# Kernel optimization log

Hardware: AMD Instinct MI355X
Metric: run time of the kernel (lower is better)

The kernel has to match this reference:

```python
import jax, jax.numpy as jnp
import numpy as np

T, B, D, R = 1024, 32, 1024, 128

def _orth_cols(key, n, r):
    # mimic torch QR-based orthogonal init: Q[:, :r] of a random [n, r] matrix
    a = jax.random.normal(key, (n, r), dtype=jnp.float32)
    q, _ = jnp.linalg.qr(a)
    return q[:, :r]

def setup_inputs() -> dict:
    key = jax.random.key(0)
    ks = jax.random.split(key, 8)
    x = jax.random.normal(ks[0], (T, B, D), dtype=jnp.float32)
    z = jax.random.normal(ks[1], (T, B, D), dtype=jnp.float32)
    h0 = jnp.zeros((B, D), dtype=jnp.float32)
    U_h = _orth_cols(ks[2], D, R)
    V_h = _orth_cols(ks[3], D, R).T  # [R, D] with orthonormal rows
    U_x = _orth_cols(ks[4], D, R)
    V_x = _orth_cols(ks[5], D, R).T
    s_h = jnp.ones((R,), dtype=jnp.float32)
    s_x = jnp.ones((R,), dtype=jnp.float32)
    b = jnp.zeros((D,), dtype=jnp.float32)
    return {"x": x, "z": z, "h0": h0, "U_h": U_h, "V_h": V_h, "s_h": s_h,
            "U_x": U_x, "V_x": V_x, "s_x": s_x, "b": b}

def reference(x, z, h0, U_h, V_h, s_h, U_x, V_x, s_x, b):
    # Precompute V_x @ x_t for all timesteps: [T, B, R]
    Vx_all = jnp.einsum('tbd,rd->tbr', x, V_x)
    Ux_all = jnp.einsum('tbr,dr->tbd', s_x * Vx_all, U_x)  # input branch, no recurrence

    def step(h_prev, inp):
        Ux_t, z_t = inp
        Vh = h_prev @ V_h.T                 # [B, R]
        Uh = (s_h * Vh) @ U_h.T             # [B, D]
        h_new = jnp.tanh(Uh + Ux_t + b)
        out_t = h_new * jax.nn.silu(z_t)
        return h_new, (h_new, out_t)

    _, (hs, output) = jax.lax.scan(step, h0, (Ux_all, z))
    h = jnp.concatenate([h0[None], hs], axis=0)  # [T+1, B, D]
    return output, h
```

## Files before the change

### kernel.cpp

```cpp
#include <hip/hip_runtime.h>
#include <cstdint>

#define T_STEPS 1024
#define BATCH   32
#define DIM     1024
#define RANK    128
#define BD      (BATCH*DIM)
#define TBD     ((size_t)T_STEPS*BD)

typedef _Float16 half2v __attribute__((ext_vector_type(2)));

__device__ __forceinline__ float dot2f(uint32_t a, uint32_t b, float acc) {
#if __has_builtin(__builtin_amdgcn_fdot2)
  return __builtin_amdgcn_fdot2(__builtin_bit_cast(half2v, a),
                                __builtin_bit_cast(half2v, b), acc, false);
#else
  half2v xx = __builtin_bit_cast(half2v, a);
  half2v yy = __builtin_bit_cast(half2v, b);
  return acc + (float)xx[0]*(float)yy[0] + (float)xx[1]*(float)yy[1];
#endif
}

__device__ __forceinline__ float dot2x4(uint4 w, uint4 h, float acc) {
  acc = dot2f(w.x, h.x, acc); acc = dot2f(w.y, h.y, acc);
  acc = dot2f(w.z, h.z, acc); acc = dot2f(w.w, h.w, acc);
  return acc;
}

__device__ __forceinline__ uint16_t f16b(float x) {
  _Float16 h = (_Float16)x;
  return __builtin_bit_cast(unsigned short, h);
}
__device__ __forceinline__ uint32_t pack2(float a, float b) {
  return (uint32_t)f16b(a) | ((uint32_t)f16b(b) << 16);
}
__device__ __forceinline__ float fast_tanh(float x) {
  float e = __expf(2.0f*x);
  return 1.0f - 2.0f/(e + 1.0f);
}
__device__ __forceinline__ float fast_silu(float zz) {
  return zz / (1.0f + __expf(-zz));
}

__device__ __forceinline__ void pin4(uint4 &v) {
  asm volatile("" : "+v"(v.x), "+v"(v.y), "+v"(v.z), "+v"(v.w));
}

template<int K>
__device__ __forceinline__ uint32_t qbcast(uint32_t v) {
  return (uint32_t)__builtin_amdgcn_mov_dpp((int)v, K*0x55, 0xf, 0xf, true);
}
template<int K>
__device__ __forceinline__ uint4 qbcast4(uint4 v) {
  uint4 r;
  r.x = qbcast<K>(v.x); r.y = qbcast<K>(v.y);
  r.z = qbcast<K>(v.z); r.w = qbcast<K>(v.w);
  return r;
}
template<int CTRL>
__device__ __forceinline__ float dpp_xorf(float v) {
  int t = __builtin_amdgcn_mov_dpp(__builtin_bit_cast(int, v), CTRL, 0xf, 0xf, true);
  return __builtin_bit_cast(float, t);
}

__device__ __forceinline__ void lds_barrier() {
  asm volatile("s_waitcnt lgkmcnt(0)" ::: "memory");
  __builtin_amdgcn_s_barrier();
  __builtin_amdgcn_sched_barrier(0);
}

__global__ void prep_kernel(const float* __restrict__ Uh, const float* __restrict__ Vh,
                            const float* __restrict__ sh, const float* __restrict__ Ux,
                            const float* __restrict__ Vx, const float* __restrict__ sx,
                            const float* __restrict__ h0, uint32_t* __restrict__ ws32,
                            float* __restrict__ hout) {
  int i = blockIdx.x*blockDim.x + threadIdx.x;
  int n = gridDim.x*blockDim.x;
  for (int p = i; p < 65536; p += n) {
    int r = p >> 9, dp = p & 511;
    ws32[p] = pack2(Vh[r*1024 + 2*dp], Vh[r*1024 + 2*dp + 1]);
  }
  for (int p = i; p < 65536; p += n) {
    int d = p >> 6, k = p & 63;
    uint32_t w = pack2(Uh[d*128 + k]      * sh[k],
                       Uh[d*128 + 64 + k] * sh[64 + k]);
    if (k < 52) {
      int J = (k >> 2) + 13*(d & 1);
      ws32[65536 + J*2048 + (d >> 1)*4 + (k & 3)] = w;
    } else {
      ws32[118784 + d*12 + (k - 52)] = w;
    }
  }
  for (int p = i; p < 65536; p += n) {
    int r = p >> 9, dp = p & 511;
    ws32[131072 + p] = pack2(Vx[r*1024 + 2*dp], Vx[r*1024 + 2*dp + 1]);
  }
  for (int p = i; p < 65536; p += n) {
    int d = p >> 6, rp = p & 63;
    ws32[196608 + p] = pack2(Ux[d*128 + 2*rp]   * sx[2*rp],
                             Ux[d*128 + 2*rp+1] * sx[2*rp+1]);
  }
  for (int p = i; p < BD; p += n) hout[p] = h0[p];
}

__global__ __launch_bounds__(512, 4) void inp_kernel(
    const float* __restrict__ x, const uint32_t* __restrict__ ws32,
    const float* __restrict__ bias, float* __restrict__ hout) {
  const int t = blockIdx.x;
  const int l = threadIdx.x;
  __shared__ __attribute__((aligned(16))) uint32_t xs[32*516];
  __shared__ __attribute__((aligned(16))) uint16_t svx[BATCH*RANK];

  const float4* xg = (const float4*)(x + (size_t)t*BD);
  #pragma unroll
  for (int k = 0; k < 16; k++) {
    int i = l + 512*k;
    float4 v = xg[i];
    int bb = i >> 8;
    int d4 = i & 255;
    xs[bb*516 + d4*2]     = pack2(v.x, v.y);
    xs[bb*516 + d4*2 + 1] = pack2(v.z, v.w);
  }
  __syncthreads();

  const int q4 = l & 3;
  const int r  = l >> 2;
  const uint4* wrow = (const uint4*)(ws32 + 131072 + r*512);
  float acc0[8], acc1[8];
  #pragma unroll
  for (int bi = 0; bi < 8; bi++) { acc0[bi] = 0.f; acc1[bi] = 0.f; }
  #pragma unroll 4
  for (int J = 0; J < 128; J += 2) {
    uint4 w0 = wrow[J];
    uint4 w1 = wrow[J+1];
    #pragma unroll
    for (int bi = 0; bi < 8; bi++) {
      const uint4* xrow = (const uint4*)(xs + (4*bi + q4)*516);
      uint4 h0v = xrow[J];
      acc0[bi] = dot2f(w0.x, h0v.x, acc0[bi]);
      acc0[bi] = dot2f(w0.y, h0v.y, acc0[bi]);
      acc0[bi] = dot2f(w0.z, h0v.z, acc0[bi]);
      acc0[bi] = dot2f(w0.w, h0v.w, acc0[bi]);
      uint4 h1v = xrow[J+1];
      acc1[bi] = dot2f(w1.x, h1v.x, acc1[bi]);
      acc1[bi] = dot2f(w1.y, h1v.y, acc1[bi]);
      acc1[bi] = dot2f(w1.z, h1v.z, acc1[bi]);
      acc1[bi] = dot2f(w1.w, h1v.w, acc1[bi]);
    }
  }
  #pragma unroll
  for (int bi = 0; bi < 8; bi++)
    svx[(4*bi + q4)*RANK + r] = f16b(acc0[bi] + acc1[bi]);
  __syncthreads();

  const uint4* svx4 = (const uint4*)svx;
  float accb[BATCH];
  #pragma unroll 1
  for (int dd = 0; dd < 2; dd++) {
    int d = l + dd*512;
    const uint4* urow = (const uint4*)(ws32 + 196608 + d*64);
    #pragma unroll
    for (int bi = 0; bi < BATCH; bi++) accb[bi] = 0.f;
    #pragma unroll
    for (int RP = 0; RP < 16; RP++) {
      uint4 w = urow[RP];
      #pragma unroll
      for (int bi = 0; bi < BATCH; bi++) {
        uint4 sv = svx4[bi*16 + RP];
        accb[bi] = dot2f(w.x, sv.x, accb[bi]);
        accb[bi] = dot2f(w.y, sv.y, accb[bi]);
        accb[bi] = dot2f(w.z, sv.z, accb[bi]);
        accb[bi] = dot2f(w.w, sv.w, accb[bi]);
      }
    }
    float bv = bias[d];
    float* cslot = hout + (size_t)(t+1)*BD + d;
    #pragma unroll
    for (int bi = 0; bi < BATCH; bi++)
      cslot[(size_t)bi*DIM] = accb[bi] + bv;
  }
}

__global__ __attribute__((amdgpu_flat_work_group_size(512, 512),
                          amdgpu_waves_per_eu(2, 2)))
void rec_kernel(
    const uint32_t* __restrict__ ws32, const float* __restrict__ z,
    float* __restrict__ outb) {
  const int b  = blockIdx.x;
  const int l  = threadIdx.x;
  const int W  = l & 31;
  const int R8 = l >> 5;
  const int m  = l & 3;
  float* hout = outb + TBD;
  const uint4* vhw4  = (const uint4*)ws32;
  const uint4* uqs4  = (const uint4*)(ws32 + 65536);
  const uint4* ures4 = (const uint4*)(ws32 + 118784);

  __shared__ __attribute__((aligned(16))) uint4    vlds[6144];
  __shared__ __attribute__((aligned(16))) uint4    ulds[3072];
  __shared__ __attribute__((aligned(16))) uint4    hbuf[32*5];
  __shared__ __attribute__((aligned(16))) uint32_t svh32[64];

  uint4 vw[5][4];
  #pragma unroll
  for (int r = 0; r < 5; r++) {
    #pragma unroll
    for (int c = 0; c < 4; c++) vw[r][c] = vhw4[(8*R8 + r)*128 + W*4 + c];
  }
  #pragma unroll
  for (int r = 0; r < 5; r++) {
    #pragma unroll
    for (int c = 0; c < 4; c++) pin4(vw[r][c]);
  }
  #pragma unroll
  for (int rr = 0; rr < 3; rr++) {
    #pragma unroll
    for (int c = 0; c < 4; c++)
      vlds[R8*384 + rr*128 + c*32 + W] = vhw4[(8*R8 + 5 + rr)*128 + W*4 + c];
  }
  #pragma unroll
  for (int j = 0; j < 3; j++) {
    ulds[j*512 + l]     = ures4[(2*l)*3 + j];
    ulds[(3+j)*512 + l] = ures4[(2*l+1)*3 + j];
  }
  uint4 uq0[13], uq1[13];
  #pragma unroll
  for (int J = 0; J < 13; J++) {
    uq0[J] = uqs4[J*512 + l];
    uq1[J] = uqs4[(13+J)*512 + l];
  }
  {
    const float2 v = ((const float2*)(hout + (size_t)b*DIM))[l];
    ((uint32_t*)hbuf)[20*(l>>4) + (l&15)] = pack2(v.x, v.y);
  }
  __syncthreads();

  const float2* zp2 = (const float2*)(z + (size_t)b*DIM) + l;
  float2*       cp2 = (float2*)(hout + BD + (size_t)b*DIM) + l;
  float2*       op2 = (float2*)(outb + (size_t)b*DIM) + l;
  const uint4*  hb4  = hbuf + W*5;
  const uint4*  svh4 = (const uint4*)svh32;
  const int vbase = R8*384;

  #pragma unroll 1
  for (int t = 0; t < T_STEPS; t++) {
    float2 cc = *cp2;
    float2 zz = *zp2;

    float a[8] = {0.f,0.f,0.f,0.f,0.f,0.f,0.f,0.f};
    #pragma unroll
    for (int c = 0; c < 4; c++) {
      uint4 hvc = hb4[c];
      uint4 vA = vlds[vbase + c*32 + W];
      uint4 vB = vlds[vbase + 128 + c*32 + W];
      uint4 vC = vlds[vbase + 256 + c*32 + W];
      a[0] = dot2x4(vw[0][c], hvc, a[0]);
      a[1] = dot2x4(vw[1][c], hvc, a[1]);
      a[2] = dot2x4(vw[2][c], hvc, a[2]);
      a[3] = dot2x4(vw[3][c], hvc, a[3]);
      a[4] = dot2x4(vw[4][c], hvc, a[4]);
      a[5] = dot2x4(vA, hvc, a[5]);
      a[6] = dot2x4(vB, hvc, a[6]);
      a[7] = dot2x4(vC, hvc, a[7]);
    }
    float b4[4];
    {
      const bool s0 = (W & 1);
      #pragma unroll
      for (int i = 0; i < 4; i++) {
        float keep = s0 ? a[2*i+1] : a[2*i];
        float send = s0 ? a[2*i]   : a[2*i+1];
        b4[i] = keep + dpp_xorf<0xB1>(send);
      }
    }
    float c2[2];
    {
      const bool s1 = (W >> 1) & 1;
      #pragma unroll
      for (int i = 0; i < 2; i++) {
        float keep = s1 ? b4[2*i+1] : b4[2*i];
        float send = s1 ? b4[2*i]   : b4[2*i+1];
        c2[i] = keep + dpp_xorf<0x4E>(send);
      }
    }
    float s;
    {
      const bool s2 = (W >> 2) & 1;
      float keep = s2 ? c2[1] : c2[0];
      float send = s2 ? c2[0] : c2[1];
      s = keep + __shfl_xor(send, 4);
    }
    s += __shfl_xor(s, 8);
    s += __shfl_xor(s, 16);
    if (W < 8) {
      int row = 8*R8 + W;
      int idx = ((row & 63) << 1) | (row >> 6);
      ((uint16_t*)svh32)[idx] = f16b(s);
    }
    lds_barrier();

    float p0 = 0.f, p1 = 0.f;
    {
      uint4 svm = svh4[m];
      uint4 sv;
      sv = qbcast4<0>(svm); p0 = dot2x4(uq0[0], sv, p0); p1 = dot2x4(uq1[0], sv, p1);
      sv = qbcast4<1>(svm); p0 = dot2x4(uq0[1], sv, p0); p1 = dot2x4(uq1[1], sv, p1);
      sv = qbcast4<2>(svm); p0 = dot2x4(uq0[2], sv, p0); p1 = dot2x4(uq1[2], sv, p1);
      sv = qbcast4<3>(svm); p0 = dot2x4(uq0[3], sv, p0); p1 = dot2x4(uq1[3], sv, p1);
    }
    {
      uint4 svm = svh4[4 + m];
      uint4 sv;
      sv = qbcast4<0>(svm); p0 = dot2x4(uq0[4], sv, p0); p1 = dot2x4(uq1[4], sv, p1);
      sv = qbcast4<1>(svm); p0 = dot2x4(uq0[5], sv, p0); p1 = dot2x4(uq1[5], sv, p1);
      sv = qbcast4<2>(svm); p0 = dot2x4(uq0[6], sv, p0); p1 = dot2x4(uq1[6], sv, p1);
      sv = qbcast4<3>(svm); p0 = dot2x4(uq0[7], sv, p0); p1 = dot2x4(uq1[7], sv, p1);
    }
    {
      uint4 svm = svh4[8 + m];
      uint4 sv;
      sv = qbcast4<0>(svm); p0 = dot2x4(uq0[8],  sv, p0); p1 = dot2x4(uq1[8],  sv, p1);
      sv = qbcast4<1>(svm); p0 = dot2x4(uq0[9],  sv, p0); p1 = dot2x4(uq1[9],  sv, p1);
      sv = qbcast4<2>(svm); p0 = dot2x4(uq0[10], sv, p0); p1 = dot2x4(uq1[10], sv, p1);
      sv = qbcast4<3>(svm); p0 = dot2x4(uq0[11], sv, p0); p1 = dot2x4(uq1[11], sv, p1);
    }
    {
      uint4 u0b = ulds[0*512 + l], u0c = ulds[1*512 + l], u0d = ulds[2*512 + l];
      uint4 u1b = ulds[3*512 + l], u1c = ulds[4*512 + l], u1d = ulds[5*512 + l];
      uint4 svm = svh4[12 + m];
      uint4 sv;
      sv = qbcast4<0>(svm); p0 = dot2x4(uq0[12], sv, p0); p1 = dot2x4(uq1[12], sv, p1);
      sv = qbcast4<1>(svm); p0 = dot2x4(u0b, sv, p0); p1 = dot2x4(u1b, sv, p1);
      sv = qbcast4<2>(svm); p0 = dot2x4(u0c, sv, p0); p1 = dot2x4(u1c, sv, p1);
      sv = qbcast4<3>(svm); p0 = dot2x4(u0d, sv, p0); p1 = dot2x4(u1d, sv, p1);
    }

    float hv0 = fast_tanh(p0 + cc.x);
    float hv1 = fast_tanh(p1 + cc.y);
    *cp2 = make_float2(hv0, hv1);
    ((uint32_t*)hbuf)[20*(l>>4) + (l&15)] = pack2(hv0, hv1);
    *op2 = make_float2(hv0 * fast_silu(zz.x), hv1 * fast_silu(zz.y));
    lds_barrier();

    cp2 += BD/2; zp2 += BD/2; op2 += BD/2;
  }
}

extern "C" void kernel_launch(void* const* d_in, const int* in_sizes, int n_in,
                              void* d_out, int out_size, void* d_ws, size_t ws_size,
                              hipStream_t stream) {
  const float* x  = (const float*)d_in[0];
  const float* z  = (const float*)d_in[1];
  const float* h0 = (const float*)d_in[2];
  const float* Uh = (const float*)d_in[3];
  const float* Vh = (const float*)d_in[4];
  const float* sh = (const float*)d_in[5];
  const float* Ux = (const float*)d_in[6];
  const float* Vx = (const float*)d_in[7];
  const float* sx = (const float*)d_in[8];
  const float* bb = (const float*)d_in[9];
  float* outb = (float*)d_out;
  uint32_t* ws32 = (uint32_t*)d_ws;

  prep_kernel<<<512, 256, 0, stream>>>(Uh, Vh, sh, Ux, Vx, sx, h0, ws32, outb + TBD);
  inp_kernel<<<T_STEPS, 512, 0, stream>>>(x, ws32, bb, outb + TBD);
  rec_kernel<<<BATCH, 512, 0, stream>>>(ws32, z, outb);
}
```

Measured before the change: 2.468 ms.

## Fuse input projection and recurrence into one persistent kernel with per-step flags

Merges the input-projection kernel and the recurrent kernel into a single launch. Blocks 0-31 run the recurrence while the other 224 blocks compute the input branch per timestep and publish completion through global release/acquire flags, so the recurrence can start before the whole input projection finishes. The recurrent loop also prefetches the next step's input term and replaces the DPP quad-broadcast with direct LDS reads of the reduced vector. The scheme relies on all 256 blocks being co-resident; otherwise the spin-waits could deadlock. It also adds polling traffic on the flags.

```diff
diff --git a/kernel.cpp b/kernel.cpp
--- a/kernel.cpp
+++ b/kernel.cpp
@@ -7,6 +7,7 @@
 #define RANK    128
 #define BD      (BATCH*DIM)
 #define TBD     ((size_t)T_STEPS*BD)
+#define WSP_FLAG 262144
 
 typedef _Float16 half2v __attribute__((ext_vector_type(2)));
 
@@ -46,17 +47,6 @@
   asm volatile("" : "+v"(v.x), "+v"(v.y), "+v"(v.z), "+v"(v.w));
 }
 
-template<int K>
-__device__ __forceinline__ uint32_t qbcast(uint32_t v) {
-  return (uint32_t)__builtin_amdgcn_mov_dpp((int)v, K*0x55, 0xf, 0xf, true);
-}
-template<int K>
-__device__ __forceinline__ uint4 qbcast4(uint4 v) {
-  uint4 r;
-  r.x = qbcast<K>(v.x); r.y = qbcast<K>(v.y);
-  r.z = qbcast<K>(v.z); r.w = qbcast<K>(v.w);
-  return r;
-}
 template<int CTRL>
 __device__ __forceinline__ float dpp_xorf(float v) {
   int t = __builtin_amdgcn_mov_dpp(__builtin_bit_cast(int, v), CTRL, 0xf, 0xf, true);
@@ -101,248 +91,263 @@
                              Ux[d*128 + 2*rp+1] * sx[2*rp+1]);
   }
   for (int p = i; p < BD; p += n) hout[p] = h0[p];
-}
-
-__global__ __launch_bounds__(512, 4) void inp_kernel(
-    const float* __restrict__ x, const uint32_t* __restrict__ ws32,
-    const float* __restrict__ bias, float* __restrict__ hout) {
-  const int t = blockIdx.x;
-  const int l = threadIdx.x;
-  __shared__ __attribute__((aligned(16))) uint32_t xs[32*516];
-  __shared__ __attribute__((aligned(16))) uint16_t svx[BATCH*RANK];
-
-  const float4* xg = (const float4*)(x + (size_t)t*BD);
-  #pragma unroll
-  for (int k = 0; k < 16; k++) {
-    int i = l + 512*k;
-    float4 v = xg[i];
-    int bb = i >> 8;
-    int d4 = i & 255;
-    xs[bb*516 + d4*2]     = pack2(v.x, v.y);
-    xs[bb*516 + d4*2 + 1] = pack2(v.z, v.w);
-  }
-  __syncthreads();
-
-  const int q4 = l & 3;
-  const int r  = l >> 2;
-  const uint4* wrow = (const uint4*)(ws32 + 131072 + r*512);
-  float acc0[8], acc1[8];
-  #pragma unroll
-  for (int bi = 0; bi < 8; bi++) { acc0[bi] = 0.f; acc1[bi] = 0.f; }
-  #pragma unroll 4
-  for (int J = 0; J < 128; J += 2) {
-    uint4 w0 = wrow[J];
-    uint4 w1 = wrow[J+1];
-    #pragma unroll
-    for (int bi = 0; bi < 8; bi++) {
-      const uint4* xrow = (const uint4*)(xs + (4*bi + q4)*516);
-      uint4 h0v = xrow[J];
-      acc0[bi] = dot2f(w0.x, h0v.x, acc0[bi]);
-      acc0[bi] = dot2f(w0.y, h0v.y, acc0[bi]);
-      acc0[bi] = dot2f(w0.z, h0v.z, acc0[bi]);
-      acc0[bi] = dot2f(w0.w, h0v.w, acc0[bi]);
-      uint4 h1v = xrow[J+1];
-      acc1[bi] = dot2f(w1.x, h1v.x, acc1[bi]);
-      acc1[bi] = dot2f(w1.y, h1v.y, acc1[bi]);
-      acc1[bi] = dot2f(w1.z, h1v.z, acc1[bi]);
-      acc1[bi] = dot2f(w1.w, h1v.w, acc1[bi]);
-    }
-  }
-  #pragma unroll
-  for (int bi = 0; bi < 8; bi++)
-    svx[(4*bi + q4)*RANK + r] = f16b(acc0[bi] + acc1[bi]);
-  __syncthreads();
-
-  const uint4* svx4 = (const uint4*)svx;
-  float accb[BATCH];
-  #pragma unroll 1
-  for (int dd = 0; dd < 2; dd++) {
-    int d = l + dd*512;
-    const uint4* urow = (const uint4*)(ws32 + 196608 + d*64);
-    #pragma unroll
-    for (int bi = 0; bi < BATCH; bi++) accb[bi] = 0.f;
-    #pragma unroll
-    for (int RP = 0; RP < 16; RP++) {
-      uint4 w = urow[RP];
-      #pragma unroll
-      for (int bi = 0; bi < BATCH; bi++) {
-        uint4 sv = svx4[bi*16 + RP];
-        accb[bi] = dot2f(w.x, sv.x, accb[bi]);
-        accb[bi] = dot2f(w.y, sv.y, accb[bi]);
-        accb[bi] = dot2f(w.z, sv.z, accb[bi]);
-        accb[bi] = dot2f(w.w, sv.w, accb[bi]);
-      }
-    }
-    float bv = bias[d];
-    float* cslot = hout + (size_t)(t+1)*BD + d;
-    #pragma unroll
-    for (int bi = 0; bi < BATCH; bi++)
-      cslot[(size_t)bi*DIM] = accb[bi] + bv;
-  }
+  for (int p = i; p < 1056; p += n) ws32[WSP_FLAG + p] = 0;
 }
 
 __global__ __attribute__((amdgpu_flat_work_group_size(512, 512),
                           amdgpu_waves_per_eu(2, 2)))
-void rec_kernel(
-    const uint32_t* __restrict__ ws32, const float* __restrict__ z,
-    float* __restrict__ outb) {
-  const int b  = blockIdx.x;
-  const int l  = threadIdx.x;
-  const int W  = l & 31;
-  const int R8 = l >> 5;
-  const int m  = l & 3;
+void fused_kernel(uint32_t* __restrict__ ws32, const float* __restrict__ x,
+                  const float* __restrict__ z, const float* __restrict__ bias,
+                  float* __restrict__ outb) {
+  __shared__ __attribute__((aligned(16))) uint8_t smem[150272];
+  const int g = blockIdx.x;
+  const int l = threadIdx.x;
   float* hout = outb + TBD;
-  const uint4* vhw4  = (const uint4*)ws32;
-  const uint4* uqs4  = (const uint4*)(ws32 + 65536);
-  const uint4* ures4 = (const uint4*)(ws32 + 118784);
-
-  __shared__ __attribute__((aligned(16))) uint4    vlds[6144];
-  __shared__ __attribute__((aligned(16))) uint4    ulds[3072];
-  __shared__ __attribute__((aligned(16))) uint4    hbuf[32*5];
-  __shared__ __attribute__((aligned(16))) uint32_t svh32[64];
-
-  uint4 vw[5][4];
-  #pragma unroll
-  for (int r = 0; r < 5; r++) {
-    #pragma unroll
-    for (int c = 0; c < 4; c++) vw[r][c] = vhw4[(8*R8 + r)*128 + W*4 + c];
-  }
-  #pragma unroll
-  for (int r = 0; r < 5; r++) {
-    #pragma unroll
-    for (int c = 0; c < 4; c++) pin4(vw[r][c]);
-  }
-  #pragma unroll
-  for (int rr = 0; rr < 3; rr++) {
-    #pragma unroll
-    for (int c = 0; c < 4; c++)
-      vlds[R8*384 + rr*128 + c*32 + W] = vhw4[(8*R8 + 5 + rr)*128 + W*4 + c];
-  }
-  #pragma unroll
-  for (int j = 0; j < 3; j++) {
-    ulds[j*512 + l]     = ures4[(2*l)*3 + j];
-    ulds[(3+j)*512 + l] = ures4[(2*l+1)*3 + j];
-  }
-  uint4 uq0[13], uq1[13];
-  #pragma unroll
-  for (int J = 0; J < 13; J++) {
-    uq0[J] = uqs4[J*512 + l];
-    uq1[J] = uqs4[(13+J)*512 + l];
-  }
-  {
-    const float2 v = ((const float2*)(hout + (size_t)b*DIM))[l];
-    ((uint32_t*)hbuf)[20*(l>>4) + (l&15)] = pack2(v.x, v.y);
-  }
-  __syncthreads();
-
-  const float2* zp2 = (const float2*)(z + (size_t)b*DIM) + l;
-  float2*       cp2 = (float2*)(hout + BD + (size_t)b*DIM) + l;
-  float2*       op2 = (float2*)(outb + (size_t)b*DIM) + l;
-  const uint4*  hb4  = hbuf + W*5;
-  const uint4*  svh4 = (const uint4*)svh32;
-  const int vbase = R8*384;
-
-  #pragma unroll 1
-  for (int t = 0; t < T_STEPS; t++) {
+  uint32_t* flags = ws32 + WSP_FLAG;
+
+  if (g < 32) {
+    const int b  = g;
+    const int W  = l & 31;
+    const int R8 = l >> 5;
+    const uint4* vhw4  = (const uint4*)ws32;
+    const uint4* uqs4  = (const uint4*)(ws32 + 65536);
+    const uint4* ures4 = (const uint4*)(ws32 + 118784);
+
+    uint4*    vlds  = (uint4*)smem;
+    uint4*    ulds  = (uint4*)(smem + 98304);
+    uint32_t* hbuf  = (uint32_t*)(smem + 147456);
+    uint32_t* svh32 = (uint32_t*)(smem + 150016);
+
+    uint4 vw[5][4];
+    #pragma unroll
+    for (int r = 0; r < 5; r++) {
+      #pragma unroll
+      for (int c = 0; c < 4; c++) vw[r][c] = vhw4[(8*R8 + r)*128 + W*4 + c];
+    }
+    #pragma unroll
+    for (int r = 0; r < 5; r++) {
+      #pragma unroll
+      for (int c = 0; c < 4; c++) pin4(vw[r][c]);
+    }
+    #pragma unroll
+    for (int rr = 0; rr < 3; rr++) {
+      #pragma unroll
+      for (int c = 0; c < 4; c++)
+        vlds[R8*384 + rr*128 + c*32 + W] = vhw4[(8*R8 + 5 + rr)*128 + W*4 + c];
+    }
+    #pragma unroll
+    for (int j = 0; j < 3; j++) {
+      ulds[j*512 + l]     = ures4[(2*l)*3 + j];
+      ulds[(3+j)*512 + l] = ures4[(2*l+1)*3 + j];
+    }
+    uint4 uq0[13], uq1[13];
+    #pragma unroll
+    for (int J = 0; J < 13; J++) {
+      uq0[J] = uqs4[J*512 + l];
+      uq1[J] = uqs4[(13+J)*512 + l];
+    }
+    {
+      const float2 v = ((const float2*)(hout + (size_t)b*DIM))[l];
+      hbuf[20*(l>>4) + (l&15)] = pack2(v.x, v.y);
+    }
+    __syncthreads();
+
+    const float2* zp2 = (const float2*)(z + (size_t)b*DIM) + l;
+    float2*       cp2 = (float2*)(hout + BD + (size_t)b*DIM) + l;
+    float2*       op2 = (float2*)(outb + (size_t)b*DIM) + l;
+    const uint4*  hb4  = (const uint4*)hbuf + W*5;
+    const uint4*  svh4 = (const uint4*)svh32;
+    const int vbase = R8*384;
+
+    while (__hip_atomic_load(&flags[1], __ATOMIC_ACQUIRE,
+                             __HIP_MEMORY_SCOPE_AGENT) == 0) {}
     float2 cc = *cp2;
-    float2 zz = *zp2;
-
-    float a[8] = {0.f,0.f,0.f,0.f,0.f,0.f,0.f,0.f};
-    #pragma unroll
-    for (int c = 0; c < 4; c++) {
-      uint4 hvc = hb4[c];
-      uint4 vA = vlds[vbase + c*32 + W];
-      uint4 vB = vlds[vbase + 128 + c*32 + W];
-      uint4 vC = vlds[vbase + 256 + c*32 + W];
-      a[0] = dot2x4(vw[0][c], hvc, a[0]);
-      a[1] = dot2x4(vw[1][c], hvc, a[1]);
-      a[2] = dot2x4(vw[2][c], hvc, a[2]);
-      a[3] = dot2x4(vw[3][c], hvc, a[3]);
-      a[4] = dot2x4(vw[4][c], hvc, a[4]);
-      a[5] = dot2x4(vA, hvc, a[5]);
-      a[6] = dot2x4(vB, hvc, a[6]);
-      a[7] = dot2x4(vC, hvc, a[7]);
-    }
-    float b4[4];
-    {
-      const bool s0 = (W & 1);
-      #pragma unroll
-      for (int i = 0; i < 4; i++) {
-        float keep = s0 ? a[2*i+1] : a[2*i];
-        float send = s0 ? a[2*i]   : a[2*i+1];
-        b4[i] = keep + dpp_xorf<0xB1>(send);
-      }
-    }
-    float c2[2];
-    {
-      const bool s1 = (W >> 1) & 1;
-      #pragma unroll
-      for (int i = 0; i < 2; i++) {
-        float keep = s1 ? b4[2*i+1] : b4[2*i];
-        float send = s1 ? b4[2*i]   : b4[2*i+1];
-        c2[i] = keep + dpp_xorf<0x4E>(send);
-      }
-    }
-    float s;
-    {
-      const bool s2 = (W >> 2) & 1;
-      float keep = s2 ? c2[1] : c2[0];
-      float send = s2 ? c2[0] : c2[1];
-      s = keep + __shfl_xor(send, 4);
-    }
-    s += __shfl_xor(s, 8);
-    s += __shfl_xor(s, 16);
-    if (W < 8) {
-      int row = 8*R8 + W;
-      int idx = ((row & 63) << 1) | (row >> 6);
-      ((uint16_t*)svh32)[idx] = f16b(s);
-    }
-    lds_barrier();
-
-    float p0 = 0.f, p1 = 0.f;
-    {
-      uint4 svm = svh4[m];
-      uint4 sv;
-      sv = qbcast4<0>(svm); p0 = dot2x4(uq0[0], sv, p0); p1 = dot2x4(uq1[0], sv, p1);
-      sv = qbcast4<1>(svm); p0 = dot2x4(uq0[1], sv, p0); p1 = dot2x4(uq1[1], sv, p1);
-      sv = qbcast4<2>(svm); p0 = dot2x4(uq0[2], sv, p0); p1 = dot2x4(uq1[2], sv, p1);
-      sv = qbcast4<3>(svm); p0 = dot2x4(uq0[3], sv, p0); p1 = dot2x4(uq1[3], sv, p1);
-    }
-    {
-      uint4 svm = svh4[4 + m];
-      uint4 sv;
-      sv = qbcast4<0>(svm); p0 = dot2x4(uq0[4], sv, p0); p1 = dot2x4(uq1[4], sv, p1);
-      sv = qbcast4<1>(svm); p0 = dot2x4(uq0[5], sv, p0); p1 = dot2x4(uq1[5], sv, p1);
-      sv = qbcast4<2>(svm); p0 = dot2x4(uq0[6], sv, p0); p1 = dot2x4(uq1[6], sv, p1);
-      sv = qbcast4<3>(svm); p0 = dot2x4(uq0[7], sv, p0); p1 = dot2x4(uq1[7], sv, p1);
-    }
-    {
-      uint4 svm = svh4[8 + m];
-      uint4 sv;
-      sv = qbcast4<0>(svm); p0 = dot2x4(uq0[8],  sv, p0); p1 = dot2x4(uq1[8],  sv, p1);
-      sv = qbcast4<1>(svm); p0 = dot2x4(uq0[9],  sv, p0); p1 = dot2x4(uq1[9],  sv, p1);
-      sv = qbcast4<2>(svm); p0 = dot2x4(uq0[10], sv, p0); p1 = dot2x4(uq1[10], sv, p1);
-      sv = qbcast4<3>(svm); p0 = dot2x4(uq0[11], sv, p0); p1 = dot2x4(uq1[11], sv, p1);
-    }
-    {
-      uint4 u0b = ulds[0*512 + l], u0c = ulds[1*512 + l], u0d = ulds[2*512 + l];
-      uint4 u1b = ulds[3*512 + l], u1c = ulds[4*512 + l], u1d = ulds[5*512 + l];
-      uint4 svm = svh4[12 + m];
-      uint4 sv;
-      sv = qbcast4<0>(svm); p0 = dot2x4(uq0[12], sv, p0); p1 = dot2x4(uq1[12], sv, p1);
-      sv = qbcast4<1>(svm); p0 = dot2x4(u0b, sv, p0); p1 = dot2x4(u1b, sv, p1);
-      sv = qbcast4<2>(svm); p0 = dot2x4(u0c, sv, p0); p1 = dot2x4(u1c, sv, p1);
-      sv = qbcast4<3>(svm); p0 = dot2x4(u0d, sv, p0); p1 = dot2x4(u1d, sv, p1);
-    }
-
-    float hv0 = fast_tanh(p0 + cc.x);
-    float hv1 = fast_tanh(p1 + cc.y);
-    *cp2 = make_float2(hv0, hv1);
-    ((uint32_t*)hbuf)[20*(l>>4) + (l&15)] = pack2(hv0, hv1);
-    *op2 = make_float2(hv0 * fast_silu(zz.x), hv1 * fast_silu(zz.y));
-    lds_barrier();
-
-    cp2 += BD/2; zp2 += BD/2; op2 += BD/2;
+
+    #pragma unroll 1
+    for (int t = 0; t < T_STEPS; t++) {
+      float2 zz = *zp2;
+      float2 ccn = make_float2(0.f, 0.f);
+      if (t < T_STEPS - 1) {
+        while (__hip_atomic_load(&flags[t+2], __ATOMIC_ACQUIRE,
+                                 __HIP_MEMORY_SCOPE_AGENT) == 0) {}
+        ccn = cp2[BD/2];
+      }
+
+      float a[8] = {0.f,0.f,0.f,0.f,0.f,0.f,0.f,0.f};
+      #pragma unroll
+      for (int c = 0; c < 4; c++) {
+        uint4 hvc = hb4[c];
+        uint4 vA = vlds[vbase + c*32 + W];
+        uint4 vB = vlds[vbase + 128 + c*32 + W];
+        uint4 vC = vlds[vbase + 256 + c*32 + W];
+        a[0] = dot2x4(vw[0][c], hvc, a[0]);
+        a[1] = dot2x4(vw[1][c], hvc, a[1]);
+        a[2] = dot2x4(vw[2][c], hvc, a[2]);
+        a[3] = dot2x4(vw[3][c], hvc, a[3]);
+        a[4] = dot2x4(vw[4][c], hvc, a[4]);
+        a[5] = dot2x4(vA, hvc, a[5]);
+        a[6] = dot2x4(vB, hvc, a[6]);
+        a[7] = dot2x4(vC, hvc, a[7]);
+      }
+      float b4[4];
+      {
+        const bool s0 = (W & 1);
+        #pragma unroll
+        for (int i = 0; i < 4; i++) {
+          float keep = s0 ? a[2*i+1] : a[2*i];
+          float send = s0 ? a[2*i]   : a[2*i+1];
+          b4[i] = keep + dpp_xorf<0xB1>(send);
+        }
+      }
+      float c2[2];
+      {
+        const bool s1 = (W >> 1) & 1;
+        #pragma unroll
+        for (int i = 0; i < 2; i++) {
+          float keep = s1 ? b4[2*i+1] : b4[2*i];
+          float send = s1 ? b4[2*i]   : b4[2*i+1];
+          c2[i] = keep + dpp_xorf<0x4E>(send);
+        }
+      }
+      float s;
+      {
+        const bool s2 = (W >> 2) & 1;
+        float keep = s2 ? c2[1] : c2[0];
+        float send = s2 ? c2[0] : c2[1];
+        s = keep + __shfl_xor(send, 4);
+      }
+      s += __shfl_xor(s, 8);
+      s += __shfl_xor(s, 16);
+      if (W < 8) {
+        int row = 8*R8 + W;
+        int idx = ((row & 63) << 1) | (row >> 6);
+        ((uint16_t*)svh32)[idx] = f16b(s);
+      }
+      lds_barrier();
+
+      float p0 = 0.f, p1 = 0.f;
+      {
+        uint4 sv0 = svh4[0], sv1 = svh4[1], sv2 = svh4[2], sv3 = svh4[3];
+        p0 = dot2x4(uq0[0], sv0, p0); p1 = dot2x4(uq1[0], sv0, p1);
+        p0 = dot2x4(uq0[1], sv1, p0); p1 = dot2x4(uq1[1], sv1, p1);
+        p0 = dot2x4(uq0[2], sv2, p0); p1 = dot2x4(uq1[2], sv2, p1);
+        p0 = dot2x4(uq0[3], sv3, p0); p1 = dot2x4(uq1[3], sv3, p1);
+      }
+      {
+        uint4 sv0 = svh4[4], sv1 = svh4[5], sv2 = svh4[6], sv3 = svh4[7];
+        p0 = dot2x4(uq0[4], sv0, p0); p1 = dot2x4(uq1[4], sv0, p1);
+        p0 = dot2x4(uq0[5], sv1, p0); p1 = dot2x4(uq1[5], sv1, p1);
+        p0 = dot2x4(uq0[6], sv2, p0); p1 = dot2x4(uq1[6], sv2, p1);
+        p0 = dot2x4(uq0[7], sv3, p0); p1 = dot2x4(uq1[7], sv3, p1);
+      }
+      {
+        uint4 sv0 = svh4[8], sv1 = svh4[9], sv2 = svh4[10], sv3 = svh4[11];
+        p0 = dot2x4(uq0[8],  sv0, p0); p1 = dot2x4(uq1[8],  sv0, p1);
+        p0 = dot2x4(uq0[9],  sv1, p0); p1 = dot2x4(uq1[9],  sv1, p1);
+        p0 = dot2x4(uq0[10], sv2, p0); p1 = dot2x4(uq1[10], sv2, p1);
+        p0 = dot2x4(uq0[11], sv3, p0); p1 = dot2x4(uq1[11], sv3, p1);
+      }
+      {
+        uint4 sv0 = svh4[12], sv1 = svh4[13], sv2 = svh4[14], sv3 = svh4[15];
+        uint4 u0b = ulds[0*512 + l], u0c = ulds[1*512 + l], u0d = ulds[2*512 + l];
+        uint4 u1b = ulds[3*512 + l], u1c = ulds[4*512 + l], u1d = ulds[5*512 + l];
+        p0 = dot2x4(uq0[12], sv0, p0); p1 = dot2x4(uq1[12], sv0, p1);
+        p0 = dot2x4(u0b, sv1, p0); p1 = dot2x4(u1b, sv1, p1);
+        p0 = dot2x4(u0c, sv2, p0); p1 = dot2x4(u1c, sv2, p1);
+        p0 = dot2x4(u0d, sv3, p0); p1 = dot2x4(u1d, sv3, p1);
+      }
+
+      float hv0 = fast_tanh(p0 + cc.x);
+      float hv1 = fast_tanh(p1 + cc.y);
+      *cp2 = make_float2(hv0, hv1);
+      hbuf[20*(l>>4) + (l&15)] = pack2(hv0, hv1);
+      *op2 = make_float2(hv0 * fast_silu(zz.x), hv1 * fast_silu(zz.y));
+      lds_barrier();
+
+      cc = ccn;
+      cp2 += BD/2; zp2 += BD/2; op2 += BD/2;
+    }
+  } else {
+    uint32_t* xs  = (uint32_t*)smem;
+    uint16_t* svx = (uint16_t*)(smem + 66048);
+
+    const int j = g - 32;
+    #pragma unroll 1
+    for (int t = j; t < T_STEPS; t += 224) {
+      const float4* xg = (const float4*)(x + (size_t)t*BD);
+      #pragma unroll
+      for (int k = 0; k < 16; k++) {
+        int i = l + 512*k;
+        float4 v = xg[i];
+        int bb = i >> 8;
+        int d4 = i & 255;
+        xs[bb*516 + d4*2]     = pack2(v.x, v.y);
+        xs[bb*516 + d4*2 + 1] = pack2(v.z, v.w);
+      }
+      __syncthreads();
+
+      const int q4 = l & 3;
+      const int r  = l >> 2;
+      const uint4* wrow = (const uint4*)(ws32 + 131072 + r*512);
+      float acc0[8], acc1[8];
+      #pragma unroll
+      for (int bi = 0; bi < 8; bi++) { acc0[bi] = 0.f; acc1[bi] = 0.f; }
+      #pragma unroll 4
+      for (int J = 0; J < 128; J += 2) {
+        uint4 w0 = wrow[J];
+        uint4 w1 = wrow[J+1];
+        #pragma unroll
+        for (int bi = 0; bi < 8; bi++) {
+          const uint4* xrow = (const uint4*)(xs + (4*bi + q4)*516);
+          uint4 h0v = xrow[J];
+          acc0[bi] = dot2f(w0.x, h0v.x, acc0[bi]);
+          acc0[bi] = dot2f(w0.y, h0v.y, acc0[bi]);
+          acc0[bi] = dot2f(w0.z, h0v.z, acc0[bi]);
+          acc0[bi] = dot2f(w0.w, h0v.w, acc0[bi]);
+          uint4 h1v = xrow[J+1];
+          acc1[bi] = dot2f(w1.x, h1v.x, acc1[bi]);
+          acc1[bi] = dot2f(w1.y, h1v.y, acc1[bi]);
+          acc1[bi] = dot2f(w1.z, h1v.z, acc1[bi]);
+          acc1[bi] = dot2f(w1.w, h1v.w, acc1[bi]);
+        }
+      }
+      #pragma unroll
+      for (int bi = 0; bi < 8; bi++)
+        svx[(4*bi + q4)*RANK + r] = f16b(acc0[bi] + acc1[bi]);
+      __syncthreads();
+
+      const uint4* svx4 = (const uint4*)svx;
+      float accb[BATCH];
+      #pragma unroll 1
+      for (int dd = 0; dd < 2; dd++) {
+        int d = l + dd*512;
+        const uint4* urow = (const uint4*)(ws32 + 196608 + d*64);
+        #pragma unroll
+        for (int bi = 0; bi < BATCH; bi++) accb[bi] = 0.f;
+        #pragma unroll
+        for (int RP = 0; RP < 16; RP++) {
+          uint4 w = urow[RP];
+          #pragma unroll
+          for (int bi = 0; bi < BATCH; bi++) {
+            uint4 sv = svx4[bi*16 + RP];
+            accb[bi] = dot2f(w.x, sv.x, accb[bi]);
+            accb[bi] = dot2f(w.y, sv.y, accb[bi]);
+            accb[bi] = dot2f(w.z, sv.z, accb[bi]);
+            accb[bi] = dot2f(w.w, sv.w, accb[bi]);
+          }
+        }
+        float bv = bias[d];
+        float* cslot = hout + (size_t)(t+1)*BD + d;
+        #pragma unroll
+        for (int bi = 0; bi < BATCH; bi++)
+          cslot[(size_t)bi*DIM] = accb[bi] + bv;
+      }
+      __syncthreads();
+      if (l == 0)
+        __hip_atomic_store(&flags[t+1], 1u, __ATOMIC_RELEASE,
+                           __HIP_MEMORY_SCOPE_AGENT);
+      __syncthreads();
+    }
   }
 }
 
@@ -363,6 +368,5 @@
   uint32_t* ws32 = (uint32_t*)d_ws;
 
   prep_kernel<<<512, 256, 0, stream>>>(Uh, Vh, sh, Ux, Vx, sx, h0, ws32, outb + TBD);
-  inp_kernel<<<T_STEPS, 512, 0, stream>>>(x, ws32, bb, outb + TBD);
-  rec_kernel<<<BATCH, 512, 0, stream>>>(ws32, z, outb);
-}
+  fused_kernel<<<256, 512, 0, stream>>>(ws32, x, z, bb, outb);
+}
```

After: 2.752 ms. 11.5% more time.

## Register-tile input projection, coalesce U_x layout, replace DPP broadcasts with LDS reads

Applied to the files above, without the earlier changes.

The V_x projection in the input kernel is rewritten so each thread computes a 4-rank by 2-batch register tile. It streams weight rows directly and reuses each loaded x vector across four ranks. The U_x weights are re-laid out in the prep kernel so consecutive threads read consecutive uint4s, which coalesces the second matmul's weight loads. In the recurrent step, the quad DPP broadcasts of the rank vector are replaced by uniform LDS broadcast reads. That removes VALU mov_dpp work but issues four LDS loads per block instead of one, and leaves a small dead DPP statement behind.

```diff
diff --git a/kernel.cpp b/kernel.cpp
--- a/kernel.cpp
+++ b/kernel.cpp
@@ -46,17 +46,6 @@
   asm volatile("" : "+v"(v.x), "+v"(v.y), "+v"(v.z), "+v"(v.w));
 }
 
-template<int K>
-__device__ __forceinline__ uint32_t qbcast(uint32_t v) {
-  return (uint32_t)__builtin_amdgcn_mov_dpp((int)v, K*0x55, 0xf, 0xf, true);
-}
-template<int K>
-__device__ __forceinline__ uint4 qbcast4(uint4 v) {
-  uint4 r;
-  r.x = qbcast<K>(v.x); r.y = qbcast<K>(v.y);
-  r.z = qbcast<K>(v.z); r.w = qbcast<K>(v.w);
-  return r;
-}
 template<int CTRL>
 __device__ __forceinline__ float dpp_xorf(float v) {
   int t = __builtin_amdgcn_mov_dpp(__builtin_bit_cast(int, v), CTRL, 0xf, 0xf, true);
@@ -96,9 +85,10 @@
     ws32[131072 + p] = pack2(Vx[r*1024 + 2*dp], Vx[r*1024 + 2*dp + 1]);
   }
   for (int p = i; p < 65536; p += n) {
-    int d = p >> 6, rp = p & 63;
-    ws32[196608 + p] = pack2(Ux[d*128 + 2*rp]   * sx[2*rp],
-                             Ux[d*128 + 2*rp+1] * sx[2*rp+1]);
+    int d = p >> 6, k = p & 63;
+    uint32_t w = pack2(Ux[d*128 + 2*k]   * sx[2*k],
+                       Ux[d*128 + 2*k+1] * sx[2*k+1]);
+    ws32[196608 + (d >> 9)*32768 + (k >> 2)*2048 + (d & 511)*4 + (k & 3)] = w;
   }
   for (int p = i; p < BD; p += n) hout[p] = h0[p];
 }
@@ -109,7 +99,7 @@
   const int t = blockIdx.x;
   const int l = threadIdx.x;
   __shared__ __attribute__((aligned(16))) uint32_t xs[32*516];
-  __shared__ __attribute__((aligned(16))) uint16_t svx[BATCH*RANK];
+  __shared__ __attribute__((aligned(16))) uint32_t svx[32*64];
 
   const float4* xg = (const float4*)(x + (size_t)t*BD);
   #pragma unroll
@@ -123,34 +113,30 @@
   }
   __syncthreads();
 
-  const int q4 = l & 3;
-  const int r  = l >> 2;
-  const uint4* wrow = (const uint4*)(ws32 + 131072 + r*512);
-  float acc0[8], acc1[8];
-  #pragma unroll
-  for (int bi = 0; bi < 8; bi++) { acc0[bi] = 0.f; acc1[bi] = 0.f; }
-  #pragma unroll 4
-  for (int J = 0; J < 128; J += 2) {
-    uint4 w0 = wrow[J];
-    uint4 w1 = wrow[J+1];
-    #pragma unroll
-    for (int bi = 0; bi < 8; bi++) {
-      const uint4* xrow = (const uint4*)(xs + (4*bi + q4)*516);
-      uint4 h0v = xrow[J];
-      acc0[bi] = dot2f(w0.x, h0v.x, acc0[bi]);
-      acc0[bi] = dot2f(w0.y, h0v.y, acc0[bi]);
-      acc0[bi] = dot2f(w0.z, h0v.z, acc0[bi]);
-      acc0[bi] = dot2f(w0.w, h0v.w, acc0[bi]);
-      uint4 h1v = xrow[J+1];
-      acc1[bi] = dot2f(w1.x, h1v.x, acc1[bi]);
-      acc1[bi] = dot2f(w1.y, h1v.y, acc1[bi]);
-      acc1[bi] = dot2f(w1.z, h1v.z, acc1[bi]);
-      acc1[bi] = dot2f(w1.w, h1v.w, acc1[bi]);
-    }
-  }
-  #pragma unroll
-  for (int bi = 0; bi < 8; bi++)
-    svx[(4*bi + q4)*RANK + r] = f16b(acc0[bi] + acc1[bi]);
+  const int rq = l >> 4;
+  const int bq = l & 15;
+  const uint4* xr0 = (const uint4*)(xs + bq*516);
+  const uint4* xr1 = (const uint4*)(xs + (bq+16)*516);
+  const uint4* wr0 = (const uint4*)(ws32 + 131072 + (4*rq    )*512);
+  const uint4* wr1 = (const uint4*)(ws32 + 131072 + (4*rq + 1)*512);
+  const uint4* wr2 = (const uint4*)(ws32 + 131072 + (4*rq + 2)*512);
+  const uint4* wr3 = (const uint4*)(ws32 + 131072 + (4*rq + 3)*512);
+  float a00=0.f,a01=0.f,a10=0.f,a11=0.f,a20=0.f,a21=0.f,a30=0.f,a31=0.f;
+  #pragma unroll 2
+  for (int J = 0; J < 128; J++) {
+    uint4 x0 = xr0[J];
+    uint4 x1 = xr1[J];
+    uint4 w0 = wr0[J];
+    uint4 w1 = wr1[J];
+    uint4 w2 = wr2[J];
+    uint4 w3 = wr3[J];
+    a00 = dot2x4(w0, x0, a00); a01 = dot2x4(w0, x1, a01);
+    a10 = dot2x4(w1, x0, a10); a11 = dot2x4(w1, x1, a11);
+    a20 = dot2x4(w2, x0, a20); a21 = dot2x4(w2, x1, a21);
+    a30 = dot2x4(w3, x0, a30); a31 = dot2x4(w3, x1, a31);
+  }
+  ((uint2*)(svx + bq*64))[rq]      = make_uint2(pack2(a00, a10), pack2(a20, a30));
+  ((uint2*)(svx + (bq+16)*64))[rq] = make_uint2(pack2(a01, a11), pack2(a21, a31));
   __syncthreads();
 
   const uint4* svx4 = (const uint4*)svx;
@@ -158,12 +144,12 @@
   #pragma unroll 1
   for (int dd = 0; dd < 2; dd++) {
     int d = l + dd*512;
-    const uint4* urow = (const uint4*)(ws32 + 196608 + d*64);
+    const uint4* uc = (const uint4*)(ws32 + 196608 + dd*32768);
     #pragma unroll
     for (int bi = 0; bi < BATCH; bi++) accb[bi] = 0.f;
     #pragma unroll
     for (int RP = 0; RP < 16; RP++) {
-      uint4 w = urow[RP];
+      uint4 w = uc[RP*512 + l];
       #pragma unroll
       for (int bi = 0; bi < BATCH; bi++) {
         uint4 sv = svx4[bi*16 + RP];
@@ -303,36 +289,37 @@
     {
       uint4 svm = svh4[m];
       uint4 sv;
-      sv = qbcast4<0>(svm); p0 = dot2x4(uq0[0], sv, p0); p1 = dot2x4(uq1[0], sv, p1);
-      sv = qbcast4<1>(svm); p0 = dot2x4(uq0[1], sv, p0); p1 = dot2x4(uq1[1], sv, p1);
-      sv = qbcast4<2>(svm); p0 = dot2x4(uq0[2], sv, p0); p1 = dot2x4(uq1[2], sv, p1);
-      sv = qbcast4<3>(svm); p0 = dot2x4(uq0[3], sv, p0); p1 = dot2x4(uq1[3], sv, p1);
-    }
-    {
-      uint4 svm = svh4[4 + m];
-      uint4 sv;
-      sv = qbcast4<0>(svm); p0 = dot2x4(uq0[4], sv, p0); p1 = dot2x4(uq1[4], sv, p1);
-      sv = qbcast4<1>(svm); p0 = dot2x4(uq0[5], sv, p0); p1 = dot2x4(uq1[5], sv, p1);
-      sv = qbcast4<2>(svm); p0 = dot2x4(uq0[6], sv, p0); p1 = dot2x4(uq1[6], sv, p1);
-      sv = qbcast4<3>(svm); p0 = dot2x4(uq0[7], sv, p0); p1 = dot2x4(uq1[7], sv, p1);
-    }
-    {
-      uint4 svm = svh4[8 + m];
-      uint4 sv;
-      sv = qbcast4<0>(svm); p0 = dot2x4(uq0[8],  sv, p0); p1 = dot2x4(uq1[8],  sv, p1);
-      sv = qbcast4<1>(svm); p0 = dot2x4(uq0[9],  sv, p0); p1 = dot2x4(uq1[9],  sv, p1);
-      sv = qbcast4<2>(svm); p0 = dot2x4(uq0[10], sv, p0); p1 = dot2x4(uq1[10], sv, p1);
-      sv = qbcast4<3>(svm); p0 = dot2x4(uq0[11], sv, p0); p1 = dot2x4(uq1[11], sv, p1);
-    }
-    {
+      sv.x = __builtin_amdgcn_mov_dpp((int)svm.x, 0*0x55, 0xf, 0xf, true);
+    }
+    {
+      uint4 sv0 = svh4[0], sv1 = svh4[1], sv2 = svh4[2], sv3 = svh4[3];
+      p0 = dot2x4(uq0[0], sv0, p0); p1 = dot2x4(uq1[0], sv0, p1);
+      p0 = dot2x4(uq0[1], sv1, p0); p1 = dot2x4(uq1[1], sv1, p1);
+      p0 = dot2x4(uq0[2], sv2, p0); p1 = dot2x4(uq1[2], sv2, p1);
+      p0 = dot2x4(uq0[3], sv3, p0); p1 = dot2x4(uq1[3], sv3, p1);
+    }
+    {
+      uint4 sv0 = svh4[4], sv1 = svh4[5], sv2 = svh4[6], sv3 = svh4[7];
+      p0 = dot2x4(uq0[4], sv0, p0); p1 = dot2x4(uq1[4], sv0, p1);
+      p0 = dot2x4(uq0[5], sv1, p0); p1 = dot2x4(uq1[5], sv1, p1);
+      p0 = dot2x4(uq0[6], sv2, p0); p1 = dot2x4(uq1[6], sv2, p1);
+      p0 = dot2x4(uq0[7], sv3, p0); p1 = dot2x4(uq1[7], sv3, p1);
+    }
+    {
+      uint4 sv0 = svh4[8], sv1 = svh4[9], sv2 = svh4[10], sv3 = svh4[11];
+      p0 = dot2x4(uq0[8],  sv0, p0); p1 = dot2x4(uq1[8],  sv0, p1);
+      p0 = dot2x4(uq0[9],  sv1, p0); p1 = dot2x4(uq1[9],  sv1, p1);
+      p0 = dot2x4(uq0[10], sv2, p0); p1 = dot2x4(uq1[10], sv2, p1);
+      p0 = dot2x4(uq0[11], sv3, p0); p1 = dot2x4(uq1[11], sv3, p1);
+    }
+    {
+      uint4 sv0 = svh4[12], sv1 = svh4[13], sv2 = svh4[14], sv3 = svh4[15];
       uint4 u0b = ulds[0*512 + l], u0c = ulds[1*512 + l], u0d = ulds[2*512 + l];
       uint4 u1b = ulds[3*512 + l], u1c = ulds[4*512 + l], u1d = ulds[5*512 + l];
-      uint4 svm = svh4[12 + m];
-      uint4 sv;
-      sv = qbcast4<0>(svm); p0 = dot2x4(uq0[12], sv, p0); p1 = dot2x4(uq1[12], sv, p1);
-      sv = qbcast4<1>(svm); p0 = dot2x4(u0b, sv, p0); p1 = dot2x4(u1b, sv, p1);
-      sv = qbcast4<2>(svm); p0 = dot2x4(u0c, sv, p0); p1 = dot2x4(u1c, sv, p1);
-      sv = qbcast4<3>(svm); p0 = dot2x4(u0d, sv, p0); p1 = dot2x4(u1d, sv, p1);
+      p0 = dot2x4(uq0[12], sv0, p0); p1 = dot2x4(uq1[12], sv0, p1);
+      p0 = dot2x4(u0b, sv1, p0); p1 = dot2x4(u1b, sv1, p1);
+      p0 = dot2x4(u0c, sv2, p0); p1 = dot2x4(u1c, sv2, p1);
+      p0 = dot2x4(u0d, sv3, p0); p1 = dot2x4(u1d, sv3, p1);
     }
 
     float hv0 = fast_tanh(p0 + cc.x);
```

After: 2.226 ms. 9.8% less time.
